# Kernel optimization log

Hardware: AMD Instinct MI355X
Metric: run time of the kernel (lower is better)

## Reference

```python
import jax, jax.numpy as jnp
import numpy as np

CHUNK, STEP, NCHUNK = 75, 25, 22
DIM, HEADS = 64, 8
BN_EPS = 1e-5


def _conv1d(x, w, b):
    # x: [N, Cin, L], w: [Cout, Cin, K] (torch layout), VALID padding, stride 1
    y = jax.lax.conv_general_dilated(x, w, (1,), 'VALID',
                                     dimension_numbers=('NCH', 'OIH', 'NCH'))
    return y + b[None, :, None]


def _bn(x, gamma, beta, mean, var):
    # inference-mode batchnorm over channel dim of [N, C, L]
    scale = gamma / jnp.sqrt(var + BN_EPS)
    return (x - mean[None, :, None]) * scale[None, :, None] + beta[None, :, None]


def _swish(x):
    return x * jax.nn.sigmoid(x)


def _encode(audio, p):
    # audio: [B, 1, L] -> overlapping chunks [B, 22, 1, 75] via gather (unfold)
    B = audio.shape[0]
    idx = np.arange(NCHUNK)[:, None] * STEP + np.arange(CHUNK)[None, :]  # [22, 75]
    x = audio[:, :, idx]                      # [B, 1, 22, 75]
    x = x.transpose(0, 2, 1, 3).reshape(B * NCHUNK, 1, CHUNK)
    x = _swish(_bn(_conv1d(x, p['w1'], p['b1']), p['g1'], p['be1'], p['m1'], p['v1']))  # [B*22,16,50]
    x = _swish(_bn(_conv1d(x, p['w2'], p['b2']), p['g2'], p['be2'], p['m2'], p['v2']))  # [B*22,32,25]
    x = _swish(_bn(_conv1d(x, p['w3'], p['b3']), p['g3'], p['be3'], p['m3'], p['v3']))  # [B*22,64,1]
    return x[:, :, 0].reshape(B, NCHUNK, DIM)  # concat over chunks == seq of 22 tokens


def _mha(feat, p):
    # per-head full-width linears (torch Linear: y = x @ W.T + b), stacked over heads
    # Wq/Wk/Wv: [H, D, D]; bq/bk/bv: [H, D]
    B, S, D = feat.shape
    Q = jnp.einsum('bsd,hed->bhse', feat, p['Wq']) + p['bq'][None, :, None, :]
    K = jnp.einsum('bsd,hed->bhse', feat, p['Wk']) + p['bk'][None, :, None, :]
    V = jnp.einsum('bsd,hed->bhse', feat, p['Wv']) + p['bv'][None, :, None, :]
    A = jax.nn.softmax(jnp.einsum('bhse,bhte->bhst', Q, K), axis=-1)  # no 1/sqrt(d) scaling in source
    O = jnp.einsum('bhst,bhte->bhse', A, V)       # [B, H, S, D]
    O = O.transpose(0, 2, 1, 3).reshape(B, S, HEADS * D)  # concat heads along feature dim
    return O @ p['Wfc'].T + p['bfc']              # [B, S, D]


def setup_inputs() -> dict:
    key = jax.random.key(0)
    ks = jax.random.split(key, 16)
    B, L = 4096, 600
    C1, C2 = DIM // 4, DIM // 2
    inp = {
        'audio_vec1': jax.random.normal(ks[0], (B, 1, L), jnp.float32),
        'audio_vec2': jax.random.normal(ks[1], (B, 1, L), jnp.float32),
        # conv stack
        'w1': jax.random.normal(ks[2], (C1, 1, 26), jnp.float32) * 0.05,
        'b1': jnp.zeros((C1,), jnp.float32),
        'g1': jnp.ones((C1,), jnp.float32), 'be1': jnp.zeros((C1,), jnp.float32),
        'm1': jnp.zeros((C1,), jnp.float32), 'v1': jnp.ones((C1,), jnp.float32),
        'w2': jax.random.normal(ks[3], (C2, C1, 26), jnp.float32) * 0.05,
        'b2': jnp.zeros((C2,), jnp.float32),
        'g2': jnp.ones((C2,), jnp.float32), 'be2': jnp.zeros((C2,), jnp.float32),
        'm2': jnp.zeros((C2,), jnp.float32), 'v2': jnp.ones((C2,), jnp.float32),
        'w3': jax.random.normal(ks[4], (DIM, C2, 25), jnp.float32) * 0.05,
        'b3': jnp.zeros((DIM,), jnp.float32),
        'g3': jnp.ones((DIM,), jnp.float32), 'be3': jnp.zeros((DIM,), jnp.float32),
        'm3': jnp.zeros((DIM,), jnp.float32), 'v3': jnp.ones((DIM,), jnp.float32),
        # attention (per-head full-width projections)
        'Wq': jax.random.normal(ks[5], (HEADS, DIM, DIM), jnp.float32) * 0.05,
        'bq': jnp.zeros((HEADS, DIM), jnp.float32),
        'Wk': jax.random.normal(ks[6], (HEADS, DIM, DIM), jnp.float32) * 0.05,
        'bk': jnp.zeros((HEADS, DIM), jnp.float32),
        'Wv': jax.random.normal(ks[7], (HEADS, DIM, DIM), jnp.float32) * 0.05,
        'bv': jnp.zeros((HEADS, DIM), jnp.float32),
        'Wfc': jax.random.normal(ks[8], (DIM, HEADS * DIM), jnp.float32) * 0.05,
        'bfc': jnp.zeros((DIM,), jnp.float32),
        # final fc
        'Wout': jax.random.normal(ks[9], (DIM, DIM), jnp.float32) * 0.05,
        'bout': jnp.zeros((DIM,), jnp.float32),
    }
    return inp


def reference(audio_vec1, audio_vec2, w1, b1, g1, be1, m1, v1,
              w2, b2, g2, be2, m2, v2, w3, b3, g3, be3, m3, v3,
              Wq, bq, Wk, bk, Wv, bv, Wfc, bfc, Wout, bout):
    p = dict(w1=w1, b1=b1, g1=g1, be1=be1, m1=m1, v1=v1,
             w2=w2, b2=b2, g2=g2, be2=be2, m2=m2, v2=v2,
             w3=w3, b3=b3, g3=g3, be3=be3, m3=m3, v3=v3,
             Wq=Wq, bq=bq, Wk=Wk, bk=bk, Wv=Wv, bv=bv, Wfc=Wfc, bfc=bfc)
    f1 = _encode(audio_vec1, p)   # [B, 22, 64]
    f2 = _encode(audio_vec2, p)
    f1 = _mha(f1, p).mean(axis=1) @ Wout.T + bout  # [B, 64]
    f2 = _mha(f2, p).mean(axis=1) @ Wout.T + bout
    return (f1, f2)
```

## Files before the change

### kernel.cpp

```cpp
#include <hip/hip_runtime.h>
#include <math.h>

#define NCHUNK 22
#define SEQLEN 600
#define BN_EPS 1e-5f

#define OFF_W1F    0
#define OFF_W2F    1024
#define OFF_W3F    14336
#define OFF_MHF    65536
#define OFF_WC     98304
#define OFF_UH     131072
#define OFF_WH     131584
#define OFF_CH     132096
#define OFF_CBIAS  132104
#define OFF_WCOMB  132168
#define OFF_FEAT   164936
#define REPACK_N   132104

typedef short bf16x8 __attribute__((ext_vector_type(8)));
typedef float f32x4 __attribute__((ext_vector_type(4)));
typedef float f32x16 __attribute__((ext_vector_type(16)));

#if __has_builtin(__builtin_amdgcn_perm)
#define PERM_HI(r0, r1) __builtin_amdgcn_perm((r1), (r0), 0x05040100u)
#define PERM_LO(r0, r1) __builtin_amdgcn_perm((r1), (r0), 0x07060302u)
#else
#define PERM_HI(r0, r1) (((r0) & 0xFFFFu) | ((r1) << 16))
#define PERM_LO(r0, r1) (((r0) >> 16) | ((r1) & 0xFFFF0000u))
#endif

__device__ __forceinline__ float swishf(float z) {
    return z / (1.f + __expf(-z));
}
__device__ __forceinline__ unsigned short bf16_rne(float f) {
    unsigned int u = __float_as_uint(f);
    return (unsigned short)((u + 0x7FFFu + ((u >> 16) & 1u)) >> 16);
}
__device__ __forceinline__ float bf16_tof(unsigned short h) {
    return __uint_as_float(((unsigned int)h) << 16);
}
__device__ __forceinline__ unsigned int pack_hl(float f) {
    unsigned int u = __float_as_uint(f);
    unsigned int h = (u + 0x7FFFu + ((u >> 16) & 1u)) >> 16;
    float r = f - __uint_as_float(h << 16);
    unsigned int v = __float_as_uint(r);
    unsigned int l = (v + 0x7FFFu + ((v >> 16) & 1u)) >> 16;
    return h | (l << 16);
}
__device__ __forceinline__ unsigned int dup_word(float f, int pat) {
    unsigned short h = bf16_rne(f);
    unsigned short v = pat ? bf16_rne(f - bf16_tof(h)) : h;
    return (unsigned int)v | ((unsigned int)v << 16);
}
__device__ __forceinline__ unsigned int frag_word(float f0, float f1, int hl) {
    unsigned short h0 = bf16_rne(f0), h1 = bf16_rne(f1);
    if (hl == 0) return (unsigned int)h0 | ((unsigned int)h1 << 16);
    unsigned short l0 = bf16_rne(f0 - bf16_tof(h0));
    unsigned short l1 = bf16_rne(f1 - bf16_tof(h1));
    return (unsigned int)l0 | ((unsigned int)l1 << 16);
}
__device__ __forceinline__ void frag_from_packed(const unsigned int* p, bf16x8& h8, bf16x8& l8) {
    unsigned int r0 = p[0], r1 = p[1], r2 = p[2], r3 = p[3];
    unsigned int r4 = p[4], r5 = p[5], r6 = p[6], r7 = p[7];
    union U { unsigned int w[4]; bf16x8 v; } H, L;
    H.w[0] = PERM_HI(r0, r1); H.w[1] = PERM_HI(r2, r3);
    H.w[2] = PERM_HI(r4, r5); H.w[3] = PERM_HI(r6, r7);
    L.w[0] = PERM_LO(r0, r1); L.w[1] = PERM_LO(r2, r3);
    L.w[2] = PERM_LO(r4, r5); L.w[3] = PERM_LO(r6, r7);
    h8 = H.v; l8 = L.v;
}

__global__ __launch_bounds__(256) void repack_kernel(
    const float* __restrict__ w1, const float* __restrict__ w2, const float* __restrict__ w3,
    const float* __restrict__ Wq, const float* __restrict__ Wk, const float* __restrict__ Wv,
    const float* __restrict__ Wfc, const float* __restrict__ Wout,
    const float* __restrict__ bq, const float* __restrict__ bk,
    float* __restrict__ ws)
{
    int tid = blockIdx.x * 256 + threadIdx.x;
    unsigned int* wsu = (unsigned int*)ws;
    if (tid < 1024) {
        int r = tid & 3, lane = (tid >> 2) & 63, pat = (tid >> 8) & 1, ph = (tid >> 9) & 1;
        int li = lane & 15, lg = lane >> 4;
        int k = ph * 16 + lg * 4 + r;
        float f = (k < 26) ? w1[li * 26 + k] : 0.f;
        wsu[OFF_W1F + tid] = dup_word(f, pat);
    }
    int t2 = tid - 1024;
    if (t2 >= 0 && t2 < 13312) {
        int r = t2 & 3, lane = (t2 >> 2) & 63, hl = (t2 >> 8) & 1, s = t2 >> 9;
        int co = lane & 31;
        int ci0 = (lane >> 5) * 8;
        float f0 = w2[co * 416 + (ci0 + 2 * r) * 26 + s];
        float f1 = w2[co * 416 + (ci0 + 2 * r + 1) * 26 + s];
        wsu[OFF_W2F + t2] = frag_word(f0, f1, hl);
    }
    int t3 = tid - 14336;
    if (t3 >= 0 && t3 < 51200) {
        int r = t3 & 3, l = (t3 >> 2) & 63, hl = (t3 >> 8) & 1;
        int nt = (t3 >> 9) & 3, s = t3 >> 11;
        int co = nt * 16 + (l & 15);
        int k0 = s * 32 + (l >> 4) * 8 + 2 * r;
        float f0 = w3[co * 800 + (k0 & 31) * 25 + (k0 >> 5)];
        float f1 = w3[co * 800 + ((k0 + 1) & 31) * 25 + ((k0 + 1) >> 5)];
        wsu[OFF_W3F + t3] = frag_word(f0, f1, hl);
    }
    int t4 = tid - 65536;
    if (t4 >= 0 && t4 < 32768) {
        int r = t4 & 3, l = (t4 >> 2) & 63, hl = (t4 >> 8) & 1;
        int nt = (t4 >> 9) & 3, ks = (t4 >> 11) & 1, h = t4 >> 12;
        int n = nt * 16 + (l & 15);
        int d0 = ks * 32 + (l >> 4) * 8 + 2 * r;
        const float* wqh = Wq + h * 4096;
        const float* wkh = Wk + h * 4096;
        float f0 = 0.f, f1 = 0.f;
        #pragma unroll 8
        for (int e = 0; e < 64; ++e) {
            float wk_en = wkh[e * 64 + n];
            f0 = fmaf(wqh[e * 64 + d0],     wk_en, f0);
            f1 = fmaf(wqh[e * 64 + d0 + 1], wk_en, f1);
        }
        wsu[OFF_MHF + t4] = frag_word(f0, f1, hl);
    }
    int t7 = tid - 98304;
    if (t7 >= 0 && t7 < 32768) {
        int k = t7 & 63, j = t7 >> 6;
        float acc = 0.f;
        #pragma unroll 8
        for (int d = 0; d < 64; ++d)
            acc = fmaf(Wfc[d * 512 + j], Wout[k * 64 + d], acc);
        ws[OFF_WCOMB + t7] = acc;
    }
    int t8 = tid - 131072;
    if (t8 >= 0 && t8 < 512) {
        int h = t8 >> 6, d = t8 & 63;
        float acc = 0.f;
        #pragma unroll 8
        for (int e = 0; e < 64; ++e) acc = fmaf(Wq[h * 4096 + e * 64 + d], bk[h * 64 + e], acc);
        ws[OFF_UH + t8] = acc;
    }
    int t9 = tid - 131584;
    if (t9 >= 0 && t9 < 512) {
        int h = t9 >> 6, d = t9 & 63;
        float acc = 0.f;
        #pragma unroll 8
        for (int e = 0; e < 64; ++e) acc = fmaf(Wk[h * 4096 + e * 64 + d], bq[h * 64 + e], acc);
        ws[OFF_WH + t9] = acc;
    }
    int t10 = tid - 132096;
    if (t10 >= 0 && t10 < 8) {
        float acc = 0.f;
        #pragma unroll 8
        for (int e = 0; e < 64; ++e) acc = fmaf(bq[t10 * 64 + e], bk[t10 * 64 + e], acc);
        ws[OFF_CH + t10] = acc;
    }
}

__global__ __launch_bounds__(256) void repack2_kernel(
    const float* __restrict__ Wv, float* __restrict__ ws)
{
    int tid = blockIdx.x * 256 + threadIdx.x;
    int k = tid & 63, j = tid >> 6;
    int h = j >> 6, d = j & 63;
    const float* wcomb = ws + OFF_WCOMB + (size_t)(h * 64) * 64 + k;
    const float* wv = Wv + h * 4096 + d;
    float acc = 0.f;
    #pragma unroll 8
    for (int e = 0; e < 64; ++e)
        acc = fmaf(wv[e * 64], wcomb[e * 64], acc);
    ws[OFF_WC + tid] = acc;
}

__global__ __launch_bounds__(64) void cbias_kernel(
    const float* __restrict__ Wfc, const float* __restrict__ Wout,
    const float* __restrict__ bfc, const float* __restrict__ bout,
    const float* __restrict__ bv, float* __restrict__ ws)
{
    __shared__ float sd_s[64];
    int t = threadIdx.x;
    float acc = 0.f;
    for (int j = 0; j < 512; ++j) acc = fmaf(bv[j], Wfc[t * 512 + j], acc);
    sd_s[t] = acc;
    __syncthreads();
    float cb = bout[t];
    #pragma unroll 8
    for (int dp = 0; dp < 64; ++dp) cb = fmaf(bfc[dp] + sd_s[dp], Wout[t * 64 + dp], cb);
    ws[OFF_CBIAS + t] = cb;
}

__global__ __launch_bounds__(256, 6) void encoder_kernel(
    const float* __restrict__ audio1, const float* __restrict__ audio2,
    const float* __restrict__ b1, const float* __restrict__ g1, const float* __restrict__ be1,
    const float* __restrict__ m1, const float* __restrict__ v1,
    const float* __restrict__ b2, const float* __restrict__ g2, const float* __restrict__ be2,
    const float* __restrict__ m2, const float* __restrict__ v2,
    const float* __restrict__ b3, const float* __restrict__ g3, const float* __restrict__ be3,
    const float* __restrict__ m3, const float* __restrict__ v3,
    float* __restrict__ ws, int B)
{
    __shared__ __align__(16) unsigned int smem[6504];
    unsigned int* a_p = smem;
    unsigned int* w2f = smem + 192;
    unsigned short* y1h16 = (unsigned short*)(smem + 2240);
    unsigned short* y1l16 = (unsigned short*)(smem + 3780);
    unsigned short* y2h16 = (unsigned short*)(smem + 2240);
    unsigned short* y2l16 = (unsigned short*)(smem + 4260);
    float* A_s  = (float*)(smem + 6280);
    float* Bc_s = (float*)(smem + 6392);

    int t = threadIdx.x;
    int blk = blockIdx.x;
    int seq = blk / 5, tile = blk - seq * 5;
    int tc = (tile == 4) ? 2 : 5;
    int nq = 25 * tc;
    int ny1 = nq + 25;
    int na = nq + 50;
    const unsigned int* wsu = (const unsigned int*)ws;
    int lane = t & 63, wid = t >> 6;
    int li = lane & 15, lg = lane >> 4;

    const float* audio = (seq < B ? audio1 + (size_t)seq * SEQLEN
                                  : audio2 + (size_t)(seq - B) * SEQLEN) + tile * 125;
    uint4 w1b[2][2];
    #pragma unroll
    for (int ph = 0; ph < 2; ++ph)
        #pragma unroll
        for (int pat = 0; pat < 2; ++pat)
            w1b[ph][pat] = *(const uint4*)(wsu + OFF_W1F + ((ph * 2 + pat) * 64 + lane) * 4);

    if (t < 192) a_p[t] = (t < na) ? pack_hl(audio[t]) : 0u;
    *(uint4*)(w2f + t * 4) = *(const uint4*)(wsu + OFF_W2F + t * 4);
    if (t < 16)       { float A = g1[t] * rsqrtf(v1[t] + BN_EPS); A_s[t] = A; Bc_s[t] = (b1[t] - m1[t]) * A + be1[t]; }
    else if (t < 48)  { int i = t - 16; float A = g2[i] * rsqrtf(v2[i] + BN_EPS); A_s[t] = A; Bc_s[t] = (b2[i] - m2[i]) * A + be2[i]; }
    else if (t < 112) { int i = t - 48; float A = g3[i] * rsqrtf(v3[i] + BN_EPS); A_s[t] = A; Bc_s[t] = (b3[i] - m3[i]) * A + be3[i]; }
    for (int i = ny1 * 10 + t; i < 1540; i += 256) {
        (smem + 2240)[i] = 0u;
        (smem + 3780)[i] = 0u;
    }
    __syncthreads();

    {
        int nMt1 = (ny1 + 15) >> 4;
        float Ai = A_s[li], Bi = Bc_s[li];
        for (int mt = wid; mt < nMt1; mt += 4) {
            f32x4 acc = {0.f, 0.f, 0.f, 0.f};
            #pragma unroll
            for (int ph = 0; ph < 2; ++ph) {
                const unsigned int* ap = a_p + mt * 16 + li + ph * 16 + lg * 4;
                union { unsigned int w[4]; bf16x8 v; } A;
                A.w[0] = ap[0]; A.w[1] = ap[1]; A.w[2] = ap[2]; A.w[3] = ap[3];
                bf16x8 b0 = *(const bf16x8*)&w1b[ph][0];
                bf16x8 b1 = *(const bf16x8*)&w1b[ph][1];
                acc = __builtin_amdgcn_mfma_f32_16x16x32_bf16(A.v, b0, acc, 0, 0, 0);
                acc = __builtin_amdgcn_mfma_f32_16x16x32_bf16(A.v, b1, acc, 0, 0, 0);
            }
            #pragma unroll
            for (int r = 0; r < 4; ++r) {
                int p = mt * 16 + lg * 4 + r;
                if (p < ny1) {
                    float f = swishf(fmaf(acc[r], Ai, Bi));
                    unsigned short hh = bf16_rne(f);
                    unsigned short ll = bf16_rne(f - bf16_tof(hh));
                    y1h16[p * 20 + li] = hh;
                    y1l16[p * 20 + li] = ll;
                }
            }
        }
    }
    __syncthreads();

    int row0 = wid * 32 + (lane & 31);
    int ci0 = (lane >> 5) * 8;
    f32x16 acc2;
    #pragma unroll
    for (int r = 0; r < 16; ++r) acc2[r] = 0.f;

    for (int stg = 0; stg < 13; ++stg) {
        uint4 vnext;
        if (stg < 12)
            vnext = *(const uint4*)(wsu + OFF_W2F + (stg + 1) * 1024 + t * 4);
        const unsigned int* cur = w2f + (stg & 1) * 1024;
        #pragma unroll
        for (int half = 0; half < 2; ++half) {
            int s = stg * 2 + half;
            bf16x8 bh = *(const bf16x8*)(cur + half * 512 + lane * 4);
            bf16x8 bl = *(const bf16x8*)(cur + half * 512 + 256 + lane * 4);
            const unsigned short* hp = y1h16 + (row0 + s) * 20 + ci0;
            const unsigned short* lp = y1l16 + (row0 + s) * 20 + ci0;
            union { uint2 u[2]; bf16x8 v; } Ah, Al;
            Ah.u[0] = *(const uint2*)hp; Ah.u[1] = *(const uint2*)(hp + 4);
            Al.u[0] = *(const uint2*)lp; Al.u[1] = *(const uint2*)(lp + 4);
            acc2 = __builtin_amdgcn_mfma_f32_32x32x16_bf16(Ah.v, bh, acc2, 0, 0, 0);
            acc2 = __builtin_amdgcn_mfma_f32_32x32x16_bf16(Al.v, bh, acc2, 0, 0, 0);
            acc2 = __builtin_amdgcn_mfma_f32_32x32x16_bf16(Ah.v, bl, acc2, 0, 0, 0);
        }
        if (stg < 12)
            *(uint4*)(w2f + ((stg + 1) & 1) * 1024 + t * 4) = vnext;
        __syncthreads();
    }
    {
        int co = lane & 31;
        float Ac = A_s[16 + co], Bc = Bc_s[16 + co];
        int rbase = 4 * (lane >> 5) + wid * 32;
        #pragma unroll
        for (int reg = 0; reg < 16; ++reg) {
            int q = rbase + (reg & 3) + 8 * (reg >> 2);
            if (q < nq) {
                int cc = q / 25, qp = q - cc * 25;
                float f = swishf(fmaf(acc2[reg], Ac, Bc));
                unsigned short hh = bf16_rne(f);
                unsigned short ll = bf16_rne(f - bf16_tof(hh));
                y2h16[cc * 808 + qp * 32 + co] = hh;
                y2l16[cc * 808 + qp * 32 + co] = ll;
            }
        }
    }
    __syncthreads();

    {
        const uint4* w3f4 = (const uint4*)(wsu + OFF_W3F);
        f32x4 acc3 = {0.f, 0.f, 0.f, 0.f};
        for (int b5 = 0; b5 < 5; ++b5) {
            uint4 BH[5], BL[5];
            #pragma unroll
            for (int i = 0; i < 5; ++i) {
                int s = b5 * 5 + i;
                BH[i] = w3f4[((s * 4 + wid) * 2 + 0) * 64 + lane];
                BL[i] = w3f4[((s * 4 + wid) * 2 + 1) * 64 + lane];
            }
            #pragma unroll
            for (int i = 0; i < 5; ++i) {
                int s = b5 * 5 + i;
                bf16x8 ah = {}, al = {};
                if (li < tc) {
                    ah = *(const bf16x8*)(y2h16 + li * 808 + s * 32 + lg * 8);
                    al = *(const bf16x8*)(y2l16 + li * 808 + s * 32 + lg * 8);
                }
                bf16x8 bh = *(const bf16x8*)&BH[i];
                bf16x8 bl = *(const bf16x8*)&BL[i];
                acc3 = __builtin_amdgcn_mfma_f32_16x16x32_bf16(ah, bh, acc3, 0, 0, 0);
                acc3 = __builtin_amdgcn_mfma_f32_16x16x32_bf16(al, bh, acc3, 0, 0, 0);
                acc3 = __builtin_amdgcn_mfma_f32_16x16x32_bf16(ah, bl, acc3, 0, 0, 0);
            }
        }
        int co = wid * 16 + li;
        float A3 = A_s[48 + co], B3 = Bc_s[48 + co];
        unsigned int* featp = (unsigned int*)ws + OFF_FEAT;
        #pragma unroll
        for (int r = 0; r < 4; ++r) {
            int cc = lg * 4 + r;
            if (cc < tc)
                featp[((size_t)(seq * NCHUNK + tile * 5 + cc)) * 64 + co]
                    = pack_hl(swishf(fmaf(acc3[r], A3, B3)));
        }
    }
}

__global__ __launch_bounds__(256, 3) void mha_kernel(
    const float* __restrict__ ws, float* __restrict__ out, int B)
{
    __shared__ __align__(16) unsigned int smem[12398];
    unsigned int* f_p = smem;
    float* f32F   = (float*)(smem + 7480);
    float* rowqc  = (float*)(smem + 10942);
    float* wh_s   = (float*)(smem + 11118);
    float* fbar_s = (float*)(smem + 11630);
    float* fred   = (float*)(smem + 12142);

    int t = threadIdx.x, b = blockIdx.x;
    int lane = t & 63, wid = t >> 6;
    int li = lane & 15, lg = lane >> 4;
    const unsigned int* wsu = (const unsigned int*)ws;
    const unsigned int* featp = wsu + OFF_FEAT + (size_t)b * 1408;
    for (int i = t; i < 1408; i += 256) {
        unsigned int w = featp[i];
        int s = i >> 6, d = i & 63;
        f_p[s * 68 + d] = w;
        f32F[s * 65 + d] = __uint_as_float(w << 16) + __uint_as_float(w & 0xFFFF0000u);
    }
    for (int i = t; i < 512; i += 256) wh_s[i] = ws[OFF_WH + i];
    __syncthreads();

    unsigned int* q_pw = smem + 1496 + wid * 1496;
    float* P      = (float*)(smem + 8910) + wid * 484;
    float* abar_w = (float*)(smem + 10846) + wid * 24;
    float* rowq_w = rowqc + wid * 44;

    if (lane < 44) {
        int hl = lane / 22, s = lane - hl * 22;
        int h = wid * 2 + hl;
        float acc = ws[OFF_CH + h];
        const float* uh = ws + OFF_UH + h * 64;
        #pragma unroll 8
        for (int d = 0; d < 64; ++d) acc = fmaf(f32F[s * 65 + d], uh[d], acc);
        rowq_w[lane] = acc;
    }

    bf16x8 fah[2][2], fal[2][2];
    #pragma unroll
    for (int mt = 0; mt < 2; ++mt)
        #pragma unroll
        for (int ks = 0; ks < 2; ++ks)
            frag_from_packed(f_p + (mt * 16 + li) * 68 + ks * 32 + lg * 8,
                             fah[mt][ks], fal[mt][ks]);

    const uint4* mhf4 = (const uint4*)(wsu + OFF_MHF);

    #pragma unroll
    for (int hh = 0; hh < 2; ++hh) {
        int h = wid * 2 + hh;
        f32x4 a0t0 = {0,0,0,0}, a0t1 = a0t0, a0t2 = a0t0, a0t3 = a0t0;
        f32x4 a1t0 = a0t0, a1t1 = a0t0, a1t2 = a0t0, a1t3 = a0t0;
        #pragma unroll
        for (int nt = 0; nt < 4; ++nt) {
            f32x4 r0 = {0,0,0,0}, r1 = {0,0,0,0};
            #pragma unroll
            for (int ks = 0; ks < 2; ++ks) {
                uint4 bh4 = mhf4[h * 1024 + ks * 512 + nt * 128 + lane];
                uint4 bl4 = mhf4[h * 1024 + ks * 512 + nt * 128 + 64 + lane];
                bf16x8 bh = *(const bf16x8*)&bh4;
                bf16x8 bl = *(const bf16x8*)&bl4;
                r0 = __builtin_amdgcn_mfma_f32_16x16x32_bf16(fah[0][ks], bh, r0, 0, 0, 0);
                r0 = __builtin_amdgcn_mfma_f32_16x16x32_bf16(fal[0][ks], bh, r0, 0, 0, 0);
                r0 = __builtin_amdgcn_mfma_f32_16x16x32_bf16(fah[0][ks], bl, r0, 0, 0, 0);
                r1 = __builtin_amdgcn_mfma_f32_16x16x32_bf16(fah[1][ks], bh, r1, 0, 0, 0);
                r1 = __builtin_amdgcn_mfma_f32_16x16x32_bf16(fal[1][ks], bh, r1, 0, 0, 0);
                r1 = __builtin_amdgcn_mfma_f32_16x16x32_bf16(fah[1][ks], bl, r1, 0, 0, 0);
            }
            if (nt == 0) { a0t0 = r0; a1t0 = r1; }
            else if (nt == 1) { a0t1 = r0; a1t1 = r1; }
            else if (nt == 2) { a0t2 = r0; a1t2 = r1; }
            else { a0t3 = r0; a1t3 = r1; }
        }
        #pragma unroll
        for (int nt = 0; nt < 4; ++nt) {
            int col = nt * 16 + li;
            float wv = wh_s[h * 64 + col];
            f32x4 r0 = (nt == 0) ? a0t0 : (nt == 1) ? a0t1 : (nt == 2) ? a0t2 : a0t3;
            f32x4 r1 = (nt == 0) ? a1t0 : (nt == 1) ? a1t1 : (nt == 2) ? a1t2 : a1t3;
            #pragma unroll
            for (int r = 0; r < 4; ++r) {
                int row0 = lg * 4 + r;
                q_pw[row0 * 68 + col] = pack_hl(r0[r] + wv);
                int row1 = 16 + row0;
                if (row1 < 22) q_pw[row1 * 68 + col] = pack_hl(r1[r] + wv);
            }
        }
        #pragma unroll
        for (int mt = 0; mt < 2; ++mt) {
            bf16x8 tqh0, tql0, tqh1, tql1;
            frag_from_packed(q_pw + (mt * 16 + li) * 68 + 0 * 32 + lg * 8, tqh0, tql0);
            frag_from_packed(q_pw + (mt * 16 + li) * 68 + 1 * 32 + lg * 8, tqh1, tql1);
            #pragma unroll
            for (int ntile = 0; ntile < 2; ++ntile) {
                f32x4 sacc = {0, 0, 0, 0};
                sacc = __builtin_amdgcn_mfma_f32_16x16x32_bf16(tqh0, fah[ntile][0], sacc, 0, 0, 0);
                sacc = __builtin_amdgcn_mfma_f32_16x16x32_bf16(tql0, fah[ntile][0], sacc, 0, 0, 0);
                sacc = __builtin_amdgcn_mfma_f32_16x16x32_bf16(tqh0, fal[ntile][0], sacc, 0, 0, 0);
                sacc = __builtin_amdgcn_mfma_f32_16x16x32_bf16(tqh1, fah[ntile][1], sacc, 0, 0, 0);
                sacc = __builtin_amdgcn_mfma_f32_16x16x32_bf16(tql1, fah[ntile][1], sacc, 0, 0, 0);
                sacc = __builtin_amdgcn_mfma_f32_16x16x32_bf16(tqh1, fal[ntile][1], sacc, 0, 0, 0);
                int u = ntile * 16 + li;
                #pragma unroll
                for (int r = 0; r < 4; ++r) {
                    int s = mt * 16 + lg * 4 + r;
                    if (s < 22 && u < 22)
                        P[s * 22 + u] = sacc[r] + rowq_w[hh * 22 + s];
                }
            }
        }
        {
            int r2 = lane >> 1, c2 = lane & 1;
            float pm = -1e30f, psum = 0.f;
            if (lane < 44) {
                #pragma unroll
                for (int j = 0; j < 11; ++j) pm = fmaxf(pm, P[r2 * 22 + c2 * 11 + j]);
            }
            float m = fmaxf(__shfl(pm, 2 * lane), __shfl(pm, 2 * lane + 1));
            float rm = __shfl(m, r2);
            if (lane < 44) {
                #pragma unroll
                for (int j = 0; j < 11; ++j) {
                    int idx = r2 * 22 + c2 * 11 + j;
                    float ev = __expf(P[idx] - rm);
                    P[idx] = ev;
                    psum += ev;
                }
            }
            float sum = __shfl(psum, 2 * lane) + __shfl(psum, 2 * lane + 1);
            if (lane < 22) abar_w[lane] = 1.f / sum;
            if (lane < 22) {
                float a = 0.f;
                #pragma unroll
                for (int s = 0; s < 22; ++s) a += P[s * 22 + lane] * abar_w[s];
                abar_w[lane] = a * (1.f / 22.f);
            }
            float acc = 0.f;
            #pragma unroll
            for (int u = 0; u < 22; ++u) acc = fmaf(abar_w[u], f32F[u * 65 + lane], acc);
            fbar_s[h * 64 + lane] = acc;
        }
    }
    __syncthreads();
    {
        int d = t & 63, part = t >> 6;
        const float* wc = ws + OFF_WC;
        float acc = 0.f;
        for (int j = part * 128; j < part * 128 + 128; ++j)
            acc = fmaf(fbar_s[j], wc[j * 64 + d], acc);
        fred[part * 64 + d] = acc;
    }
    __syncthreads();
    if (t < 64)
        out[(size_t)b * 64 + t] = ws[OFF_CBIAS + t]
            + fred[t] + fred[64 + t] + fred[128 + t] + fred[192 + t];
}

extern "C" void kernel_launch(void* const* d_in, const int* in_sizes, int n_in,
                              void* d_out, int out_size, void* d_ws, size_t ws_size,
                              hipStream_t stream) {
    const float* audio1 = (const float*)d_in[0];
    const float* audio2 = (const float*)d_in[1];
    const float* w1   = (const float*)d_in[2];
    const float* b1   = (const float*)d_in[3];
    const float* g1   = (const float*)d_in[4];
    const float* be1  = (const float*)d_in[5];
    const float* m1   = (const float*)d_in[6];
    const float* v1   = (const float*)d_in[7];
    const float* w2   = (const float*)d_in[8];
    const float* b2   = (const float*)d_in[9];
    const float* g2   = (const float*)d_in[10];
    const float* be2  = (const float*)d_in[11];
    const float* m2   = (const float*)d_in[12];
    const float* v2   = (const float*)d_in[13];
    const float* w3   = (const float*)d_in[14];
    const float* b3   = (const float*)d_in[15];
    const float* g3   = (const float*)d_in[16];
    const float* be3  = (const float*)d_in[17];
    const float* m3   = (const float*)d_in[18];
    const float* v3   = (const float*)d_in[19];
    const float* Wq   = (const float*)d_in[20];
    const float* bq   = (const float*)d_in[21];
    const float* Wk   = (const float*)d_in[22];
    const float* bk   = (const float*)d_in[23];
    const float* Wv   = (const float*)d_in[24];
    const float* bv   = (const float*)d_in[25];
    const float* Wfc  = (const float*)d_in[26];
    const float* bfc  = (const float*)d_in[27];
    const float* Wout = (const float*)d_in[28];
    const float* bout = (const float*)d_in[29];

    float* ws  = (float*)d_ws;
    float* out = (float*)d_out;
    int B = in_sizes[0] / SEQLEN;
    int nseq = 2 * B;

    repack_kernel<<<(REPACK_N + 255) / 256, 256, 0, stream>>>(
        w1, w2, w3, Wq, Wk, Wv, Wfc, Wout, bq, bk, ws);
    repack2_kernel<<<128, 256, 0, stream>>>(Wv, ws);
    cbias_kernel<<<1, 64, 0, stream>>>(Wfc, Wout, bfc, bout, bv, ws);
    encoder_kernel<<<nseq * 5, 256, 0, stream>>>(audio1, audio2,
        b1, g1, be1, m1, v1,
        b2, g2, be2, m2, v2,
        b3, g3, be3, m3, v3,
        ws, B);
    mha_kernel<<<nseq, 256, 0, stream>>>(ws, out, B);
}
```

Baseline: 863.1 us.

## Stream conv2 weights directly into registers and split Q scratch into hi/lo planes

In the encoder kernel, the conv2 weight fragments are now loaded from global memory straight into registers, with a register-level prefetch of the next stage. This replaces the double-buffered LDS staging and removes the per-stage __syncthreads, which shrinks encoder shared memory and may allow more resident blocks. In the attention kernel, the packed hi/lo Q scratch is written as separate bf16 planes so MFMA fragments can be read with plain vector loads instead of being unpacked. The cost is more global/L2 traffic per wave, since each wave reloads the weights, plus extra register pressure. The split Q planes also rely on the second plane fitting inside the existing shared allocation.

```diff
diff --git a/kernel.cpp b/kernel.cpp
--- a/kernel.cpp
+++ b/kernel.cpp
@@ -199,15 +199,14 @@
     const float* __restrict__ m3, const float* __restrict__ v3,
     float* __restrict__ ws, int B)
 {
-    __shared__ __align__(16) unsigned int smem[6504];
+    __shared__ __align__(16) unsigned int smem[4456];
     unsigned int* a_p = smem;
-    unsigned int* w2f = smem + 192;
-    unsigned short* y1h16 = (unsigned short*)(smem + 2240);
-    unsigned short* y1l16 = (unsigned short*)(smem + 3780);
-    unsigned short* y2h16 = (unsigned short*)(smem + 2240);
-    unsigned short* y2l16 = (unsigned short*)(smem + 4260);
-    float* A_s  = (float*)(smem + 6280);
-    float* Bc_s = (float*)(smem + 6392);
+    unsigned short* y1h16 = (unsigned short*)(smem + 192);
+    unsigned short* y1l16 = (unsigned short*)(smem + 1732);
+    unsigned short* y2h16 = (unsigned short*)(smem + 192);
+    unsigned short* y2l16 = (unsigned short*)(smem + 2212);
+    float* A_s  = (float*)(smem + 4232);
+    float* Bc_s = (float*)(smem + 4344);
 
     int t = threadIdx.x;
     int blk = blockIdx.x;
@@ -230,13 +229,12 @@
             w1b[ph][pat] = *(const uint4*)(wsu + OFF_W1F + ((ph * 2 + pat) * 64 + lane) * 4);
 
     if (t < 192) a_p[t] = (t < na) ? pack_hl(audio[t]) : 0u;
-    *(uint4*)(w2f + t * 4) = *(const uint4*)(wsu + OFF_W2F + t * 4);
     if (t < 16)       { float A = g1[t] * rsqrtf(v1[t] + BN_EPS); A_s[t] = A; Bc_s[t] = (b1[t] - m1[t]) * A + be1[t]; }
     else if (t < 48)  { int i = t - 16; float A = g2[i] * rsqrtf(v2[i] + BN_EPS); A_s[t] = A; Bc_s[t] = (b2[i] - m2[i]) * A + be2[i]; }
     else if (t < 112) { int i = t - 48; float A = g3[i] * rsqrtf(v3[i] + BN_EPS); A_s[t] = A; Bc_s[t] = (b3[i] - m3[i]) * A + be3[i]; }
     for (int i = ny1 * 10 + t; i < 1540; i += 256) {
-        (smem + 2240)[i] = 0u;
-        (smem + 3780)[i] = 0u;
+        (smem + 192)[i] = 0u;
+        (smem + 1732)[i] = 0u;
     }
     __syncthreads();
 
@@ -275,30 +273,38 @@
     f32x16 acc2;
     #pragma unroll
     for (int r = 0; r < 16; ++r) acc2[r] = 0.f;
-
-    for (int stg = 0; stg < 13; ++stg) {
-        uint4 vnext;
-        if (stg < 12)
-            vnext = *(const uint4*)(wsu + OFF_W2F + (stg + 1) * 1024 + t * 4);
-        const unsigned int* cur = w2f + (stg & 1) * 1024;
-        #pragma unroll
-        for (int half = 0; half < 2; ++half) {
-            int s = stg * 2 + half;
-            bf16x8 bh = *(const bf16x8*)(cur + half * 512 + lane * 4);
-            bf16x8 bl = *(const bf16x8*)(cur + half * 512 + 256 + lane * 4);
-            const unsigned short* hp = y1h16 + (row0 + s) * 20 + ci0;
-            const unsigned short* lp = y1l16 + (row0 + s) * 20 + ci0;
-            union { uint2 u[2]; bf16x8 v; } Ah, Al;
-            Ah.u[0] = *(const uint2*)hp; Ah.u[1] = *(const uint2*)(hp + 4);
-            Al.u[0] = *(const uint2*)lp; Al.u[1] = *(const uint2*)(lp + 4);
-            acc2 = __builtin_amdgcn_mfma_f32_32x32x16_bf16(Ah.v, bh, acc2, 0, 0, 0);
-            acc2 = __builtin_amdgcn_mfma_f32_32x32x16_bf16(Al.v, bh, acc2, 0, 0, 0);
-            acc2 = __builtin_amdgcn_mfma_f32_32x32x16_bf16(Ah.v, bl, acc2, 0, 0, 0);
-        }
-        if (stg < 12)
-            *(uint4*)(w2f + ((stg + 1) & 1) * 1024 + t * 4) = vnext;
-        __syncthreads();
-    }
+    {
+        const uint4* w2f4 = (const uint4*)(wsu + OFF_W2F);
+        uint4 nbh0 = w2f4[(0 * 2 + 0) * 64 + lane];
+        uint4 nbl0 = w2f4[(0 * 2 + 1) * 64 + lane];
+        uint4 nbh1 = w2f4[(1 * 2 + 0) * 64 + lane];
+        uint4 nbl1 = w2f4[(1 * 2 + 1) * 64 + lane];
+        for (int stg = 0; stg < 13; ++stg) {
+            uint4 cbh0 = nbh0, cbl0 = nbl0, cbh1 = nbh1, cbl1 = nbl1;
+            if (stg < 12) {
+                int s2 = stg * 2 + 2, s3 = stg * 2 + 3;
+                nbh0 = w2f4[(s2 * 2 + 0) * 64 + lane];
+                nbl0 = w2f4[(s2 * 2 + 1) * 64 + lane];
+                nbh1 = w2f4[(s3 * 2 + 0) * 64 + lane];
+                nbl1 = w2f4[(s3 * 2 + 1) * 64 + lane];
+            }
+            #pragma unroll
+            for (int half = 0; half < 2; ++half) {
+                int s = stg * 2 + half;
+                bf16x8 bh = *(const bf16x8*)(half ? &cbh1 : &cbh0);
+                bf16x8 bl = *(const bf16x8*)(half ? &cbl1 : &cbl0);
+                const unsigned short* hp = y1h16 + (row0 + s) * 20 + ci0;
+                const unsigned short* lp = y1l16 + (row0 + s) * 20 + ci0;
+                union { uint2 u[2]; bf16x8 v; } Ah, Al;
+                Ah.u[0] = *(const uint2*)hp; Ah.u[1] = *(const uint2*)(hp + 4);
+                Al.u[0] = *(const uint2*)lp; Al.u[1] = *(const uint2*)(lp + 4);
+                acc2 = __builtin_amdgcn_mfma_f32_32x32x16_bf16(Ah.v, bh, acc2, 0, 0, 0);
+                acc2 = __builtin_amdgcn_mfma_f32_32x32x16_bf16(Al.v, bh, acc2, 0, 0, 0);
+                acc2 = __builtin_amdgcn_mfma_f32_32x32x16_bf16(Ah.v, bl, acc2, 0, 0, 0);
+            }
+        }
+    }
+    __syncthreads();
     {
         int co = lane & 31;
         float Ac = A_s[16 + co], Bc = Bc_s[16 + co];
@@ -382,7 +388,8 @@
     for (int i = t; i < 512; i += 256) wh_s[i] = ws[OFF_WH + i];
     __syncthreads();
 
-    unsigned int* q_pw = smem + 1496 + wid * 1496;
+    unsigned short* qh_w = (unsigned short*)(smem + 1496 + wid * 1496);
+    unsigned short* ql_w = qh_w + 1496;
     float* P      = (float*)(smem + 8910) + wid * 484;
     float* abar_w = (float*)(smem + 10846) + wid * 24;
     float* rowq_w = rowqc + wid * 44;
@@ -442,25 +449,39 @@
             #pragma unroll
             for (int r = 0; r < 4; ++r) {
                 int row0 = lg * 4 + r;
-                q_pw[row0 * 68 + col] = pack_hl(r0[r] + wv);
+                float v0 = r0[r] + wv;
+                unsigned short h0 = bf16_rne(v0);
+                qh_w[row0 * 68 + col] = h0;
+                ql_w[row0 * 68 + col] = bf16_rne(v0 - bf16_tof(h0));
                 int row1 = 16 + row0;
-                if (row1 < 22) q_pw[row1 * 68 + col] = pack_hl(r1[r] + wv);
+                if (row1 < 22) {
+                    float v1 = r1[r] + wv;
+                    unsigned short h1 = bf16_rne(v1);
+                    qh_w[row1 * 68 + col] = h1;
+                    ql_w[row1 * 68 + col] = bf16_rne(v1 - bf16_tof(h1));
+                }
             }
         }
         #pragma unroll
         for (int mt = 0; mt < 2; ++mt) {
-            bf16x8 tqh0, tql0, tqh1, tql1;
-            frag_from_packed(q_pw + (mt * 16 + li) * 68 + 0 * 32 + lg * 8, tqh0, tql0);
-            frag_from_packed(q_pw + (mt * 16 + li) * 68 + 1 * 32 + lg * 8, tqh1, tql1);
+            union { uint2 u[2]; bf16x8 v; } Th0, Tl0, Th1, Tl1;
+            {
+                const unsigned short* hp = qh_w + (mt * 16 + li) * 68 + lg * 8;
+                const unsigned short* lp = ql_w + (mt * 16 + li) * 68 + lg * 8;
+                Th0.u[0] = *(const uint2*)hp;        Th0.u[1] = *(const uint2*)(hp + 4);
+                Tl0.u[0] = *(const uint2*)lp;        Tl0.u[1] = *(const uint2*)(lp + 4);
+                Th1.u[0] = *(const uint2*)(hp + 32); Th1.u[1] = *(const uint2*)(hp + 36);
+                Tl1.u[0] = *(const uint2*)(lp + 32); Tl1.u[1] = *(const uint2*)(lp + 36);
+            }
             #pragma unroll
             for (int ntile = 0; ntile < 2; ++ntile) {
                 f32x4 sacc = {0, 0, 0, 0};
-                sacc = __builtin_amdgcn_mfma_f32_16x16x32_bf16(tqh0, fah[ntile][0], sacc, 0, 0, 0);
-                sacc = __builtin_amdgcn_mfma_f32_16x16x32_bf16(tql0, fah[ntile][0], sacc, 0, 0, 0);
-                sacc = __builtin_amdgcn_mfma_f32_16x16x32_bf16(tqh0, fal[ntile][0], sacc, 0, 0, 0);
-                sacc = __builtin_amdgcn_mfma_f32_16x16x32_bf16(tqh1, fah[ntile][1], sacc, 0, 0, 0);
-                sacc = __builtin_amdgcn_mfma_f32_16x16x32_bf16(tql1, fah[ntile][1], sacc, 0, 0, 0);
-                sacc = __builtin_amdgcn_mfma_f32_16x16x32_bf16(tqh1, fal[ntile][1], sacc, 0, 0, 0);
+                sacc = __builtin_amdgcn_mfma_f32_16x16x32_bf16(Th0.v, fah[ntile][0], sacc, 0, 0, 0);
+                sacc = __builtin_amdgcn_mfma_f32_16x16x32_bf16(Tl0.v, fah[ntile][0], sacc, 0, 0, 0);
+                sacc = __builtin_amdgcn_mfma_f32_16x16x32_bf16(Th0.v, fal[ntile][0], sacc, 0, 0, 0);
+                sacc = __builtin_amdgcn_mfma_f32_16x16x32_bf16(Th1.v, fah[ntile][1], sacc, 0, 0, 0);
+                sacc = __builtin_amdgcn_mfma_f32_16x16x32_bf16(Tl1.v, fah[ntile][1], sacc, 0, 0, 0);
+                sacc = __builtin_amdgcn_mfma_f32_16x16x32_bf16(Th1.v, fal[ntile][1], sacc, 0, 0, 0);
                 int u = ntile * 16 + li;
                 #pragma unroll
                 for (int r = 0; r < 4; ++r) {
```

Result: slower. 888.6 us (+2.9%).
